# Optimization experiments

Hardware: AMD Instinct MI355X
Metric: run time of the kernel (lower is better)

The kernel has to match this reference:

```python
import jax, jax.numpy as jnp
import numpy as np

B, E, H, TOP_K = 4096, 64, 512, 8
NEG_INF = jnp.finfo(jnp.float32).min


def setup_inputs() -> dict:
    key = jax.random.key(0)
    ks = jax.random.split(key, 10)
    inv = lambda fan_in: 1.0 / np.sqrt(fan_in)
    return {
        "x_context": jax.random.normal(ks[0], (B, 68), dtype=jnp.float32),
        "x_q_values": jax.random.normal(ks[1], (B, E, 3), dtype=jnp.float32),
        "x_reward": jax.random.normal(ks[2], (B, E, 2), dtype=jnp.float32),
        "x_risk": jax.random.normal(ks[3], (B, E, 2), dtype=jnp.float32),
        # context_encoder: Linear(68, H)
        "Wc": jax.random.uniform(ks[4], (68, H), jnp.float32, -inv(68), inv(68)),
        "bc": jax.random.uniform(ks[5], (H,), jnp.float32, -inv(68), inv(68)),
        # expert_encoder: Linear(7, H)
        "We": jax.random.uniform(ks[6], (7, H), jnp.float32, -inv(7), inv(7)),
        "be": jax.random.uniform(ks[7], (H,), jnp.float32, -inv(7), inv(7)),
        # router_scorer: Linear(2H, 1)
        "Ws": jax.random.uniform(ks[8], (2 * H,), jnp.float32, -inv(2 * H), inv(2 * H)),
        "bs": jax.random.uniform(ks[9], (), jnp.float32, -inv(2 * H), inv(2 * H)),
    }


def reference(x_context, x_q_values, x_reward, x_risk, Wc, bc, We, be, Ws, bs):
    # context encoder: [B,68] -> [B,H]
    context_encoded = x_context @ Wc + bc
    # per-expert inputs: concat(q, reward, risk) -> [B,E,7] -> [B,E,H]
    expert_inputs = jnp.concatenate([x_q_values, x_reward, x_risk], axis=-1)
    expert_encoded = jnp.einsum("bef,fh->beh", expert_inputs, We) + be
    # scorer over concat([expert_encoded, context_expanded]): split the dot
    # product instead of materializing combined [B,E,2H] twice
    Ws_e, Ws_c = Ws[:H], Ws[H:]
    expert_logits = (
        jnp.einsum("beh,h->be", expert_encoded, Ws_e)
        + (context_encoded @ Ws_c)[:, None]
        + bs
    )  # [B,E]
    # top-k masked softmax
    topk_val, topk_idx = jax.lax.top_k(expert_logits, TOP_K)
    rows = jnp.arange(expert_logits.shape[0])[:, None]
    sparse = jnp.full_like(expert_logits, NEG_INF).at[rows, topk_idx].set(topk_val)
    gate_weights = jax.nn.softmax(sparse, axis=-1)  # [B,E]
    # gating bmm: [B,1,E] @ [B,E,3] -> [B,3]
    action_logits = jnp.einsum("be,bea->ba", gate_weights, x_q_values)
    return (action_logits, gate_weights, expert_logits)
```

## Files before the change

kernel.cpp:

```cpp
#include <hip/hip_runtime.h>
#include <cfloat>

#define NB 4096
#define NE 64
#define NH 512
#define TOPK 8

__global__ void precompute_kernel(const float* __restrict__ Wc,
                                  const float* __restrict__ bc,
                                  const float* __restrict__ We,
                                  const float* __restrict__ be,
                                  const float* __restrict__ Ws,
                                  const float* __restrict__ bs,
                                  float* __restrict__ ws) {
    int r = blockIdx.x;
    int lane = threadIdx.x;
    float partial = 0.f;
    if (r < 7) {
        const float* row = We + r * NH;
        for (int h = lane; h < NH; h += 64) partial += row[h] * Ws[h];
    } else if (r < 75) {
        const float* row = Wc + (r - 7) * NH;
        for (int h = lane; h < NH; h += 64) partial += row[h] * Ws[NH + h];
    } else {
        for (int h = lane; h < NH; h += 64)
            partial += be[h] * Ws[h] + bc[h] * Ws[NH + h];
    }
    for (int off = 32; off; off >>= 1) partial += __shfl_xor(partial, off);
    if (lane == 0) {
        if (r == 75) partial += bs[0];
        ws[r] = partial;
    }
}

__global__ __launch_bounds__(256) void router_kernel(
    const float* __restrict__ x_context,
    const float* __restrict__ x_q,
    const float* __restrict__ x_r,
    const float* __restrict__ x_k,
    const float* __restrict__ ws,
    float* __restrict__ out_action,
    float* __restrict__ out_gate,
    float* __restrict__ out_logits)
{
    __shared__ float sws[76];
    int t = threadIdx.x;
    if (t < 76) sws[t] = ws[t];
    __syncthreads();

    int lane = t & 63;
    int b = blockIdx.x * 4 + (t >> 6);

    const float* xc = x_context + (size_t)b * 68;
    float cb = xc[lane] * sws[7 + lane];
    if (lane < 4) cb += xc[64 + lane] * sws[7 + 64 + lane];
    for (int off = 32; off; off >>= 1) cb += __shfl_xor(cb, off);

    size_t be_idx = (size_t)b * NE + lane;
    float q0 = x_q[be_idx * 3 + 0];
    float q1 = x_q[be_idx * 3 + 1];
    float q2 = x_q[be_idx * 3 + 2];
    float r0 = x_r[be_idx * 2 + 0];
    float r1 = x_r[be_idx * 2 + 1];
    float k0 = x_k[be_idx * 2 + 0];
    float k1 = x_k[be_idx * 2 + 1];

    float logit = q0 * sws[0] + q1 * sws[1] + q2 * sws[2]
                + r0 * sws[3] + r1 * sws[4]
                + k0 * sws[5] + k1 * sws[6]
                + sws[75] + cb;

    out_logits[be_idx] = logit;

    float work = logit;
    bool sel = false;
    float m = 0.f;
    #pragma unroll
    for (int k = 0; k < TOPK; ++k) {
        float bv = work;
        int bi = lane;
        for (int off = 32; off; off >>= 1) {
            float ov = __shfl_xor(bv, off);
            int oi = __shfl_xor(bi, off);
            if (ov > bv || (ov == bv && oi < bi)) { bv = ov; bi = oi; }
        }
        if (k == 0) m = bv;
        if (lane == bi) { sel = true; work = -FLT_MAX; }
    }

    float e = sel ? __expf(logit - m) : 0.f;
    float denom = e;
    for (int off = 32; off; off >>= 1) denom += __shfl_xor(denom, off);
    float gate = e / denom;
    out_gate[be_idx] = gate;

    float a0 = gate * q0, a1 = gate * q1, a2 = gate * q2;
    for (int off = 32; off; off >>= 1) {
        a0 += __shfl_xor(a0, off);
        a1 += __shfl_xor(a1, off);
        a2 += __shfl_xor(a2, off);
    }
    if (lane == 0) {
        out_action[(size_t)b * 3 + 0] = a0;
        out_action[(size_t)b * 3 + 1] = a1;
        out_action[(size_t)b * 3 + 2] = a2;
    }
}

extern "C" void kernel_launch(void* const* d_in, const int* in_sizes, int n_in,
                              void* d_out, int out_size, void* d_ws, size_t ws_size,
                              hipStream_t stream) {
    const float* x_context = (const float*)d_in[0];
    const float* x_q       = (const float*)d_in[1];
    const float* x_r       = (const float*)d_in[2];
    const float* x_k       = (const float*)d_in[3];
    const float* Wc        = (const float*)d_in[4];
    const float* bc        = (const float*)d_in[5];
    const float* We        = (const float*)d_in[6];
    const float* be        = (const float*)d_in[7];
    const float* Ws        = (const float*)d_in[8];
    const float* bs        = (const float*)d_in[9];

    float* out        = (float*)d_out;
    float* out_action = out;
    float* out_gate   = out + NB * 3;
    float* out_logits = out + NB * 3 + NB * NE;
    float* wsf = (float*)d_ws;

    precompute_kernel<<<76, 64, 0, stream>>>(Wc, bc, We, be, Ws, bs, wsf);
    router_kernel<<<NB / 4, 256, 0, stream>>>(x_context, x_q, x_r, x_k, wsf,
                                              out_action, out_gate, out_logits);
}
```

Measured before the change: 85.55 us.

## Fuse coefficient precompute into router kernel and use rank-based top-k

Removes the separate precompute launch: each block recomputes the 76 folded weight coefficients itself with serial float4 dot products by single threads, then processes 8 rows per block over a 512-block grid. Top-k selection changes from 8 rounds of wave shuffle argmax to a shared-memory rank count per lane, and the softmax denominator and action sums are reduced in one fused shuffle pass. This saves a launch and the serial reduction rounds, but every block now redoes about 300 KB of weight reads with long per-thread serial loops before any row work can start.

```diff
diff --git a/kernel.cpp b/kernel.cpp
--- a/kernel.cpp
+++ b/kernel.cpp
@@ -5,105 +5,125 @@
 #define NE 64
 #define NH 512
 #define TOPK 8
+#define GRID 512
+#define ROWS_PER_BLOCK (NB / GRID)
 
-__global__ void precompute_kernel(const float* __restrict__ Wc,
-                                  const float* __restrict__ bc,
-                                  const float* __restrict__ We,
-                                  const float* __restrict__ be,
-                                  const float* __restrict__ Ws,
-                                  const float* __restrict__ bs,
-                                  float* __restrict__ ws) {
-    int r = blockIdx.x;
-    int lane = threadIdx.x;
-    float partial = 0.f;
-    if (r < 7) {
-        const float* row = We + r * NH;
-        for (int h = lane; h < NH; h += 64) partial += row[h] * Ws[h];
-    } else if (r < 75) {
-        const float* row = Wc + (r - 7) * NH;
-        for (int h = lane; h < NH; h += 64) partial += row[h] * Ws[NH + h];
-    } else {
-        for (int h = lane; h < NH; h += 64)
-            partial += be[h] * Ws[h] + bc[h] * Ws[NH + h];
-    }
-    for (int off = 32; off; off >>= 1) partial += __shfl_xor(partial, off);
-    if (lane == 0) {
-        if (r == 75) partial += bs[0];
-        ws[r] = partial;
-    }
-}
-
-__global__ __launch_bounds__(256) void router_kernel(
+__global__ __launch_bounds__(256) void moe_router_fused(
     const float* __restrict__ x_context,
     const float* __restrict__ x_q,
     const float* __restrict__ x_r,
     const float* __restrict__ x_k,
-    const float* __restrict__ ws,
+    const float* __restrict__ Wc,
+    const float* __restrict__ bc,
+    const float* __restrict__ We,
+    const float* __restrict__ be,
+    const float* __restrict__ Ws,
+    const float* __restrict__ bs,
     float* __restrict__ out_action,
     float* __restrict__ out_gate,
     float* __restrict__ out_logits)
 {
-    __shared__ float sws[76];
+    __shared__ float scoef[76];
+    __shared__ __align__(16) float sval[4][64];
+
     int t = threadIdx.x;
-    if (t < 76) sws[t] = ws[t];
+
+    if (t < 76) {
+        float acc = 0.f;
+        if (t < 7) {
+            const float4* row = (const float4*)(We + t * NH);
+            const float4* wv  = (const float4*)(Ws);
+            #pragma unroll 8
+            for (int i = 0; i < NH / 4; ++i) {
+                float4 a = row[i], b = wv[i];
+                acc += a.x*b.x + a.y*b.y + a.z*b.z + a.w*b.w;
+            }
+        } else if (t < 75) {
+            const float4* row = (const float4*)(Wc + (size_t)(t - 7) * NH);
+            const float4* wv  = (const float4*)(Ws + NH);
+            #pragma unroll 8
+            for (int i = 0; i < NH / 4; ++i) {
+                float4 a = row[i], b = wv[i];
+                acc += a.x*b.x + a.y*b.y + a.z*b.z + a.w*b.w;
+            }
+        } else {
+            const float4* b4  = (const float4*)be;
+            const float4* c4  = (const float4*)bc;
+            const float4* we4 = (const float4*)Ws;
+            const float4* wc4 = (const float4*)(Ws + NH);
+            #pragma unroll 8
+            for (int i = 0; i < NH / 4; ++i) {
+                float4 a = b4[i], w0 = we4[i], c = c4[i], w1 = wc4[i];
+                acc += a.x*w0.x + a.y*w0.y + a.z*w0.z + a.w*w0.w
+                     + c.x*w1.x + c.y*w1.y + c.z*w1.z + c.w*w1.w;
+            }
+            acc += bs[0];
+        }
+        scoef[t] = acc;
+    }
     __syncthreads();
 
     int lane = t & 63;
-    int b = blockIdx.x * 4 + (t >> 6);
+    int w    = t >> 6;
+    float* sc = sval[w];
 
-    const float* xc = x_context + (size_t)b * 68;
-    float cb = xc[lane] * sws[7 + lane];
-    if (lane < 4) cb += xc[64 + lane] * sws[7 + 64 + lane];
-    for (int off = 32; off; off >>= 1) cb += __shfl_xor(cb, off);
+    int b0 = blockIdx.x * ROWS_PER_BLOCK;
+    #pragma unroll
+    for (int it = 0; it < ROWS_PER_BLOCK / 4; ++it) {
+        int b = b0 + it * 4 + w;
 
-    size_t be_idx = (size_t)b * NE + lane;
-    float q0 = x_q[be_idx * 3 + 0];
-    float q1 = x_q[be_idx * 3 + 1];
-    float q2 = x_q[be_idx * 3 + 2];
-    float r0 = x_r[be_idx * 2 + 0];
-    float r1 = x_r[be_idx * 2 + 1];
-    float k0 = x_k[be_idx * 2 + 0];
-    float k1 = x_k[be_idx * 2 + 1];
+        const float* xc = x_context + (size_t)b * 68;
+        float cb = xc[lane] * scoef[7 + lane];
+        if (lane < 4) cb += xc[64 + lane] * scoef[71 + lane];
+        #pragma unroll
+        for (int off = 32; off; off >>= 1) cb += __shfl_xor(cb, off);
 
-    float logit = q0 * sws[0] + q1 * sws[1] + q2 * sws[2]
-                + r0 * sws[3] + r1 * sws[4]
-                + k0 * sws[5] + k1 * sws[6]
-                + sws[75] + cb;
+        size_t be_idx = (size_t)b * NE + lane;
+        float q0 = x_q[be_idx * 3 + 0];
+        float q1 = x_q[be_idx * 3 + 1];
+        float q2 = x_q[be_idx * 3 + 2];
+        float r0 = x_r[be_idx * 2 + 0];
+        float r1 = x_r[be_idx * 2 + 1];
+        float k0 = x_k[be_idx * 2 + 0];
+        float k1 = x_k[be_idx * 2 + 1];
 
-    out_logits[be_idx] = logit;
+        float logit = q0 * scoef[0] + q1 * scoef[1] + q2 * scoef[2]
+                    + r0 * scoef[3] + r1 * scoef[4]
+                    + k0 * scoef[5] + k1 * scoef[6]
+                    + scoef[75] + cb;
 
-    float work = logit;
-    bool sel = false;
-    float m = 0.f;
-    #pragma unroll
-    for (int k = 0; k < TOPK; ++k) {
-        float bv = work;
-        int bi = lane;
+        out_logits[be_idx] = logit;
+
+        sc[lane] = logit;
+        float m = -FLT_MAX;
+        int rank = 0;
+        #pragma unroll
+        for (int j = 0; j < 64; j += 4) {
+            float4 v = *(const float4*)(sc + j);
+            rank += (v.x > logit || (v.x == logit && (j + 0) < lane)) ? 1 : 0;
+            rank += (v.y > logit || (v.y == logit && (j + 1) < lane)) ? 1 : 0;
+            rank += (v.z > logit || (v.z == logit && (j + 2) < lane)) ? 1 : 0;
+            rank += (v.w > logit || (v.w == logit && (j + 3) < lane)) ? 1 : 0;
+            m = fmaxf(m, fmaxf(fmaxf(v.x, v.y), fmaxf(v.z, v.w)));
+        }
+
+        float e = (rank < TOPK) ? __expf(logit - m) : 0.f;
+        float d  = e;
+        float a0 = e * q0, a1 = e * q1, a2 = e * q2;
+        #pragma unroll
         for (int off = 32; off; off >>= 1) {
-            float ov = __shfl_xor(bv, off);
-            int oi = __shfl_xor(bi, off);
-            if (ov > bv || (ov == bv && oi < bi)) { bv = ov; bi = oi; }
+            d  += __shfl_xor(d,  off);
+            a0 += __shfl_xor(a0, off);
+            a1 += __shfl_xor(a1, off);
+            a2 += __shfl_xor(a2, off);
         }
-        if (k == 0) m = bv;
-        if (lane == bi) { sel = true; work = -FLT_MAX; }
-    }
-
-    float e = sel ? __expf(logit - m) : 0.f;
-    float denom = e;
-    for (int off = 32; off; off >>= 1) denom += __shfl_xor(denom, off);
-    float gate = e / denom;
-    out_gate[be_idx] = gate;
-
-    float a0 = gate * q0, a1 = gate * q1, a2 = gate * q2;
-    for (int off = 32; off; off >>= 1) {
-        a0 += __shfl_xor(a0, off);
-        a1 += __shfl_xor(a1, off);
-        a2 += __shfl_xor(a2, off);
-    }
-    if (lane == 0) {
-        out_action[(size_t)b * 3 + 0] = a0;
-        out_action[(size_t)b * 3 + 1] = a1;
-        out_action[(size_t)b * 3 + 2] = a2;
+        out_gate[be_idx] = e / d;
+        if (lane == 0) {
+            float inv = 1.f / d;
+            out_action[(size_t)b * 3 + 0] = a0 * inv;
+            out_action[(size_t)b * 3 + 1] = a1 * inv;
+            out_action[(size_t)b * 3 + 2] = a2 * inv;
+        }
     }
 }
 
@@ -125,9 +145,8 @@
     float* out_action = out;
     float* out_gate   = out + NB * 3;
     float* out_logits = out + NB * 3 + NB * NE;
-    float* wsf = (float*)d_ws;
 
-    precompute_kernel<<<76, 64, 0, stream>>>(Wc, bc, We, be, Ws, bs, wsf);
-    router_kernel<<<NB / 4, 256, 0, stream>>>(x_context, x_q, x_r, x_k, wsf,
-                                              out_action, out_gate, out_logits);
+    moe_router_fused<<<GRID, 256, 0, stream>>>(
+        x_context, x_q, x_r, x_k, Wc, bc, We, be, Ws, bs,
+        out_action, out_gate, out_logits);
 }
```

Measured after the change: 104.3 us. 1.22x slower.
